# Kernel tuning notes

Measured on AMD Instinct MI355X. Metric: run time of the kernel, lower is better.

## Reference

```python
import jax, jax.numpy as jnp
import numpy as np

N_NODES = 50000
N_EDGES = 500000
IN_FEATS = 64
H_FEATS = 128
NUM_CLASSES = 4
NUM_GRAPHS = 8
NODES_PER_GRAPH = N_NODES // NUM_GRAPHS


def setup_inputs() -> dict:
    key = jax.random.key(0)
    ks = jax.random.split(key, 12)
    in_feat = jax.random.normal(ks[0], (N_NODES, IN_FEATS), dtype=jnp.float32)
    e_weight = jax.random.uniform(ks[1], (N_EDGES,), dtype=jnp.float32)
    src = jax.random.randint(ks[2], (N_EDGES,), 0, N_NODES)
    dst = jax.random.randint(ks[3], (N_EDGES,), 0, N_NODES)
    batch_num_nodes = jnp.full((NUM_GRAPHS,), NODES_PER_GRAPH, dtype=jnp.int64)
    target_node = jax.random.randint(ks[4], (NUM_GRAPHS,), 0, NODES_PER_GRAPH)
    # Glorot-style init for GraphConv weights, zero bias (DGL defaults)
    def glorot(k, fan_in, fan_out):
        s = jnp.sqrt(6.0 / (fan_in + fan_out))
        return jax.random.uniform(k, (fan_in, fan_out), minval=-s, maxval=s, dtype=jnp.float32)
    W1 = glorot(ks[5], IN_FEATS, H_FEATS)
    b1 = jnp.zeros((H_FEATS,), dtype=jnp.float32)
    W2 = glorot(ks[6], H_FEATS, H_FEATS)
    b2 = jnp.zeros((H_FEATS,), dtype=jnp.float32)
    W3 = glorot(ks[7], H_FEATS, NUM_CLASSES)
    b3 = jnp.zeros((NUM_CLASSES,), dtype=jnp.float32)
    return {"in_feat": in_feat, "e_weight": e_weight, "src": src, "dst": dst,
            "batch_num_nodes": batch_num_nodes, "target_node": target_node,
            "W1": W1, "b1": b1, "W2": W2, "b2": b2, "W3": W3, "b3": b3}


def _graph_conv(h, src, dst, e_weight, W, b, out_norm, in_norm, n_nodes):
    # DGL GraphConv, norm='both', with per-edge weights:
    # h_src scaled by out_deg^-1/2, weighted sum over edges into dst,
    # scaled by in_deg^-1/2, then dense transform + bias.
    h = h * out_norm[:, None]
    msg = h[src] * e_weight[:, None]           # [E, d] gather + scale
    agg = jax.ops.segment_sum(msg, dst, num_segments=n_nodes)  # SPMM
    agg = agg * in_norm[:, None]
    return agg @ W + b


def reference(in_feat, e_weight, src, dst, batch_num_nodes, target_node,
              W1, b1, W2, b2, W3, b3):
    n = in_feat.shape[0]
    ones = jnp.ones((src.shape[0],), dtype=in_feat.dtype)
    out_deg = jnp.clip(jax.ops.segment_sum(ones, src, num_segments=n), 1.0)
    in_deg = jnp.clip(jax.ops.segment_sum(ones, dst, num_segments=n), 1.0)
    out_norm = jax.lax.rsqrt(out_deg)
    in_norm = jax.lax.rsqrt(in_deg)

    # target node offsets for batched graphs
    offsets = jnp.concatenate([jnp.zeros((1,), batch_num_nodes.dtype),
                               jnp.cumsum(batch_num_nodes)])[:-1]
    tgt = target_node + offsets

    h = jax.nn.relu(_graph_conv(in_feat, src, dst, e_weight, W1, b1, out_norm, in_norm, n))
    h = jax.nn.relu(_graph_conv(h, src, dst, e_weight, W2, b2, out_norm, in_norm, n))
    h = _graph_conv(h, src, dst, e_weight, W3, b3, out_norm, in_norm, n)
    return h[tgt]
```

## Files before the change

kernel.cpp:

```cpp
#include <hip/hip_runtime.h>

#define NND 50000
#define NED 500000
#define F0 64
#define F1 128
#define NCLS 4
#define NG 8

#define NBLK 256
#define NTHR 1024
#define EPT 2
#define NBAR 8
#define NSUB 8
#define STG 2048
#define STGN 2048
#define BMW ((NND + 31) / 32)
#define EMASK 0x7FFFFu

#define N1CAP 4096
#define N2CAP 1024
#define E1CAP 32768
#define E2CAP 8192
#define E3CAP 2048


template <typename T>
__device__ __forceinline__ void st_wt(T* p, T v) {
    __hip_atomic_store(p, v, __ATOMIC_RELAXED, __HIP_MEMORY_SCOPE_AGENT);
}

__device__ __forceinline__ bool bt(const unsigned* __restrict__ bm, int n) {
    return (bm[n >> 5] >> (n & 31)) & 1u;
}
__device__ __forceinline__ void bset(unsigned* bm, int n) {
    atomicOr(&bm[n >> 5], 1u << (n & 31));
}

__device__ __forceinline__ void load_targets(const int* __restrict__ tnode,
                                             const unsigned* __restrict__ bnn,
                                             int* t) {
    bool is64 = true;
    #pragma unroll
    for (int k = 0; k < 4; k++) if (bnn[2 * k + 1] != 0u) { is64 = false; break; }
    long long off = 0;
    #pragma unroll
    for (int g = 0; g < NG; g++) {
        t[g] = tnode[g] + (int)off;
        off += is64 ? (long long)bnn[2 * g] : (long long)(int)bnn[g];
    }
}

__device__ __forceinline__ int tgt_of(int d, const int* t) {
    int g = -1;
    #pragma unroll
    for (int k = 0; k < NG; k++) if (d == t[k]) g = k;
    return g;
}

__device__ __forceinline__ void gbar(unsigned* bar, int i) {
    asm volatile("s_waitcnt vmcnt(0)" ::: "memory");
    __syncthreads();
    if (threadIdx.x == 0) {
        unsigned* sp = bar + (size_t)(i * (NSUB + 1) + (blockIdx.x & (NSUB - 1))) * 32;
        unsigned* mp = bar + (size_t)(i * (NSUB + 1) + NSUB) * 32;
        unsigned old = __hip_atomic_fetch_add(sp, 1u, __ATOMIC_RELAXED,
                                              __HIP_MEMORY_SCOPE_AGENT);
        if (old + 1u == (unsigned)(NBLK / NSUB))
            __hip_atomic_fetch_add(mp, 1u, __ATOMIC_RELAXED, __HIP_MEMORY_SCOPE_AGENT);
        while (__hip_atomic_load(mp, __ATOMIC_RELAXED, __HIP_MEMORY_SCOPE_AGENT)
               < (unsigned)NSUB)
            __builtin_amdgcn_s_sleep(1);
    }
    __syncthreads();
}

__global__ __launch_bounds__(256) void k_init(char* ws, unsigned zw, unsigned foff, unsigned fw) {
    unsigned t = blockIdx.x * blockDim.x + threadIdx.x;
    if (t < zw) ((uint4*)ws)[t] = make_uint4(0u, 0u, 0u, 0u);
    if (t < fw) ((uint4*)(ws + foff))[t] = make_uint4(~0u, ~0u, ~0u, ~0u);
}

__global__ __launch_bounds__(NTHR) void k_main(
        const float* __restrict__ feat, const float* __restrict__ ew,
        const int* __restrict__ src, const int* __restrict__ dst,
        const int* __restrict__ tnode, const unsigned* __restrict__ bnn,
        const float* __restrict__ W1, const float* __restrict__ b1,
        const float* __restrict__ W2, const float* __restrict__ b2,
        const float* __restrict__ W3, const float* __restrict__ b3,
        float* out,
        int* idx1, int* idx2,
        unsigned* list1, unsigned* list2, unsigned* list3,
        unsigned* cnts, unsigned* incnt, unsigned* outcnt,
        unsigned* bm1, unsigned* bm2, unsigned* bmN,
        float* agg1c, float* agg2c, unsigned* bar) {
    __shared__ unsigned s_le, s_ln, s_eb, s_nb;
    __shared__ unsigned stage[STG];
    __shared__ int stageN[STGN];

    const int tid = threadIdx.x;
    const int gid = blockIdx.x * NTHR + tid;
    const int lane = tid & 63;
    int tg[NG]; load_targets(tnode, bnn, tg);

    {
        if (tid == 0) { s_le = 0; s_ln = 0; }
        __syncthreads();
        int base = gid * EPT;
        if (base < NED) {
            int2 d2 = *(const int2*)(dst + base);
            int dd[2] = {d2.x, d2.y};
            #pragma unroll
            for (int k = 0; k < 2; k++) {
                int d = dd[k];
                int g = tgt_of(d, tg);
                if (g >= 0) {
                    int e = base + k;
                    stage[atomicAdd(&s_le, 1u)] = ((unsigned)g << 19) | (unsigned)e;
                    atomicAdd(&incnt[d], 1u);
                    int s = src[e];
                    bset(bmN, s);
                    if (atomicCAS(&idx2[s], -1, -2) == -1) {
                        bset(bm2, s);
                        stageN[atomicAdd(&s_ln, 1u)] = s;
                    }
                }
            }
        }
        __syncthreads();
        if (tid == 0) {
            s_eb = s_le ? atomicAdd(&cnts[4], s_le) : 0u;
            s_nb = s_ln ? atomicAdd(&cnts[1], s_ln) : 0u;
        }
        __syncthreads();
        for (unsigned t = tid; t < s_le; t += NTHR) {
            unsigned p = s_eb + t; if (p < E3CAP) st_wt(&list3[p], stage[t]);
        }
        for (unsigned t = tid; t < s_ln; t += NTHR) {
            int s = stageN[t]; unsigned id = s_nb + t;
            st_wt(&idx2[s], id < N2CAP ? (int)id : -1);
        }
        if (blockIdx.x == 0 && tid < NG * NCLS) st_wt(&out[tid], b3[tid & 3]);
    }
    gbar(bar, 0);

    {
        if (tid == 0) { s_le = 0; s_ln = 0; }
        __syncthreads();
        int base = gid * EPT;
        if (base < NED) {
            int2 d2 = *(const int2*)(dst + base);
            int dd[2] = {d2.x, d2.y};
            #pragma unroll
            for (int k = 0; k < 2; k++) {
                int d = dd[k];
                if (bt(bm2, d)) {
                    int iv = idx2[d];
                    if (iv >= 0) {
                        int e = base + k;
                        stage[atomicAdd(&s_le, 1u)] = ((unsigned)iv << 19) | (unsigned)e;
                        if (tgt_of(d, tg) < 0) atomicAdd(&incnt[d], 1u);
                        int s = src[e];
                        bset(bmN, s);
                        if (atomicCAS(&idx1[s], -1, -2) == -1) {
                            bset(bm1, s);
                            stageN[atomicAdd(&s_ln, 1u)] = s;
                        }
                    }
                }
            }
        }
        __syncthreads();
        if (tid == 0) {
            s_eb = s_le ? atomicAdd(&cnts[3], s_le) : 0u;
            s_nb = s_ln ? atomicAdd(&cnts[0], s_ln) : 0u;
        }
        __syncthreads();
        for (unsigned t = tid; t < s_le; t += NTHR) {
            unsigned p = s_eb + t; if (p < E2CAP) st_wt(&list2[p], stage[t]);
        }
        for (unsigned t = tid; t < s_ln; t += NTHR) {
            int s = stageN[t]; unsigned id = s_nb + t;
            st_wt(&idx1[s], id < N1CAP ? (int)id : -1);
        }
    }
    gbar(bar, 1);

    {
        if (tid == 0) s_le = 0;
        __syncthreads();
        int base = gid * EPT;
        if (base < NED) {
            int2 d2 = *(const int2*)(dst + base);
            int dd[2] = {d2.x, d2.y};
            #pragma unroll
            for (int k = 0; k < 2; k++) {
                int d = dd[k];
                if (bt(bm1, d)) {
                    int iv = idx1[d];
                    if (iv >= 0) {
                        int e = base + k;
                        stage[atomicAdd(&s_le, 1u)] = ((unsigned)iv << 19) | (unsigned)e;
                        if (idx2[d] < 0 && tgt_of(d, tg) < 0) atomicAdd(&incnt[d], 1u);
                        bset(bmN, src[e]);
                    }
                }
            }
        }
        __syncthreads();
        if (tid == 0) s_eb = s_le ? atomicAdd(&cnts[2], s_le) : 0u;
        __syncthreads();
        for (unsigned t = tid; t < s_le; t += NTHR) {
            unsigned p = s_eb + t; if (p < E1CAP) st_wt(&list1[p], stage[t]);
        }
    }
    gbar(bar, 2);

    {
        int base = gid * EPT;
        if (base < NED) {
            int2 s2 = *(const int2*)(src + base);
            int ss[2] = {s2.x, s2.y};
            #pragma unroll
            for (int k = 0; k < 2; k++)
                if (bt(bmN, ss[k])) atomicAdd(&outcnt[ss[k]], 1u);
        }
    }
    gbar(bar, 3);

    {
        unsigned e1 = cnts[2]; if (e1 > E1CAP) e1 = E1CAP;
        unsigned w = (unsigned)gid >> 6;
        const unsigned nw = (NBLK * NTHR) >> 6;
        for (unsigned i = w; i < e1; i += 2 * nw) {
            unsigned pk0 = list1[i];
            unsigned j2 = i + nw;
            unsigned pk1 = (j2 < e1) ? list1[j2] : 0u;
            int e0 = pk0 & EMASK, i10 = pk0 >> 19;
            float we0 = ew[e0]; int s0 = src[e0];
            int e1i = pk1 & EMASK, i11 = pk1 >> 19;
            float we1 = 0.f; int s1 = 0;
            if (j2 < e1) { we1 = ew[e1i]; s1 = src[e1i]; }
            float wt0 = we0 * rsqrtf(fmaxf((float)outcnt[s0], 1.f));
            atomicAdd(&agg1c[(size_t)i10 * F0 + lane],
                      feat[(size_t)s0 * F0 + lane] * wt0);
            if (j2 < e1) {
                float wt1 = we1 * rsqrtf(fmaxf((float)outcnt[s1], 1.f));
                atomicAdd(&agg1c[(size_t)i11 * F0 + lane],
                          feat[(size_t)s1 * F0 + lane] * wt1);
            }
        }
    }
    gbar(bar, 4);

    {
        unsigned e2 = cnts[3]; if (e2 > E2CAP) e2 = E2CAP;
        unsigned w = (unsigned)gid >> 6;
        const unsigned nw = (NBLK * NTHR) >> 6;
        for (unsigned i = w; i < e2; i += nw) {
            unsigned pk = list2[i];
            int e = pk & EMASK, i2 = pk >> 19;
            float we = ew[e]; int s = src[e];
            int i1 = idx1[s]; if (i1 < 0) continue;
            float wt = we * rsqrtf(fmaxf((float)outcnt[s], 1.f));
            float innorm1 = rsqrtf(fmaxf((float)incnt[s], 1.f));
            float rv = agg1c[(size_t)i1 * F0 + lane];
            float acc0 = 0.f, acc1 = 0.f;
            #pragma unroll 8
            for (int k2 = 0; k2 < F0; k2++) {
                float bv = __shfl(rv, k2, 64);
                acc0 += bv * W1[k2 * F1 + lane];
                acc1 += bv * W1[k2 * F1 + lane + 64];
            }
            float h0 = fmaxf(acc0 * innorm1 + b1[lane], 0.f) * wt;
            float h1v = fmaxf(acc1 * innorm1 + b1[lane + 64], 0.f) * wt;
            atomicAdd(&agg2c[(size_t)i2 * F1 + lane], h0);
            atomicAdd(&agg2c[(size_t)i2 * F1 + lane + 64], h1v);
        }
    }
    gbar(bar, 5);

    {
        unsigned e3 = cnts[4]; if (e3 > E3CAP) e3 = E3CAP;
        unsigned w = (unsigned)gid >> 6;
        const unsigned nw = (NBLK * NTHR) >> 6;
        for (unsigned i = w; i < e3; i += nw) {
            unsigned pk = list3[i];
            int e = pk & EMASK, g = pk >> 19;
            float we = ew[e]; int s = src[e];
            int i2 = idx2[s]; if (i2 < 0) continue;
            float wt = we * rsqrtf(fmaxf((float)outcnt[s], 1.f))
                          * rsqrtf(fmaxf((float)incnt[tg[g]], 1.f));
            float innorm2 = rsqrtf(fmaxf((float)incnt[s], 1.f));
            float rv0 = agg2c[(size_t)i2 * F1 + lane];
            float rv1 = agg2c[(size_t)i2 * F1 + lane + 64];
            float acc0 = 0.f, acc1 = 0.f;
            #pragma unroll 8
            for (int k2 = 0; k2 < 64; k2++) {
                float bv = __shfl(rv0, k2, 64);
                acc0 += bv * W2[k2 * F1 + lane];
                acc1 += bv * W2[k2 * F1 + lane + 64];
            }
            #pragma unroll 8
            for (int k2 = 0; k2 < 64; k2++) {
                float bv = __shfl(rv1, k2, 64);
                acc0 += bv * W2[(k2 + 64) * F1 + lane];
                acc1 += bv * W2[(k2 + 64) * F1 + lane + 64];
            }
            float h20 = fmaxf(acc0 * innorm2 + b2[lane], 0.f);
            float h21 = fmaxf(acc1 * innorm2 + b2[lane + 64], 0.f);
            float oc0 = (h20 * W3[lane * NCLS + 0] + h21 * W3[(lane + 64) * NCLS + 0]) * wt;
            float oc1 = (h20 * W3[lane * NCLS + 1] + h21 * W3[(lane + 64) * NCLS + 1]) * wt;
            float oc2 = (h20 * W3[lane * NCLS + 2] + h21 * W3[(lane + 64) * NCLS + 2]) * wt;
            float oc3 = (h20 * W3[lane * NCLS + 3] + h21 * W3[(lane + 64) * NCLS + 3]) * wt;
            #pragma unroll
            for (int off = 32; off; off >>= 1) {
                oc0 += __shfl_down(oc0, off, 64);
                oc1 += __shfl_down(oc1, off, 64);
                oc2 += __shfl_down(oc2, off, 64);
                oc3 += __shfl_down(oc3, off, 64);
            }
            if (lane == 0) {
                atomicAdd(&out[g * NCLS + 0], oc0);
                atomicAdd(&out[g * NCLS + 1], oc1);
                atomicAdd(&out[g * NCLS + 2], oc2);
                atomicAdd(&out[g * NCLS + 3], oc3);
            }
        }
    }
}

extern "C" void kernel_launch(void* const* d_in, const int* in_sizes, int n_in,
                              void* d_out, int out_size, void* d_ws, size_t ws_size,
                              hipStream_t stream) {
    const float* in_feat = (const float*)d_in[0];
    const float* ew      = (const float*)d_in[1];
    const int*   src     = (const int*)d_in[2];
    const int*   dst     = (const int*)d_in[3];
    const unsigned* bnn  = (const unsigned*)d_in[4];
    const int*   tnode   = (const int*)d_in[5];
    const float* W1 = (const float*)d_in[6];
    const float* b1 = (const float*)d_in[7];
    const float* W2 = (const float*)d_in[8];
    const float* b2 = (const float*)d_in[9];
    const float* W3 = (const float*)d_in[10];
    const float* b3 = (const float*)d_in[11];
    float* out = (float*)d_out;
    (void)in_sizes; (void)n_in; (void)out_size; (void)ws_size;

    char* ws = (char*)d_ws;
    size_t o = 0;
    auto alloc = [&](size_t bytes) { size_t r = o; o += (bytes + 255) & ~(size_t)255; return r; };

    size_t off_outcnt = alloc((size_t)NND * 4);
    size_t off_incnt  = alloc((size_t)NND * 4);
    size_t off_cnts   = alloc(8 * 4);
    size_t off_bar    = alloc((size_t)NBAR * (NSUB + 1) * 32 * 4);
    size_t off_bm1    = alloc((size_t)BMW * 4);
    size_t off_bm2    = alloc((size_t)BMW * 4);
    size_t off_bmN    = alloc((size_t)BMW * 4);
    size_t off_agg1   = alloc((size_t)N1CAP * F0 * 4);
    size_t off_agg2   = alloc((size_t)N2CAP * F1 * 4);
    size_t zero_bytes = o;
    size_t ff_start = o;
    size_t off_idx2   = alloc((size_t)NND * 4);
    size_t off_idx1   = alloc((size_t)NND * 4);
    size_t ff_bytes = o - ff_start;
    size_t off_list3   = alloc((size_t)E3CAP * 4);
    size_t off_list2   = alloc((size_t)E2CAP * 4);
    size_t off_list1   = alloc((size_t)E1CAP * 4);

    unsigned* outcnt  = (unsigned*)(ws + off_outcnt);
    unsigned* incnt   = (unsigned*)(ws + off_incnt);
    unsigned* cnts    = (unsigned*)(ws + off_cnts);
    unsigned* bar     = (unsigned*)(ws + off_bar);
    unsigned* bm1     = (unsigned*)(ws + off_bm1);
    unsigned* bm2     = (unsigned*)(ws + off_bm2);
    unsigned* bmN     = (unsigned*)(ws + off_bmN);
    float*    agg1c   = (float*)(ws + off_agg1);
    float*    agg2c   = (float*)(ws + off_agg2);
    int*      idx2    = (int*)(ws + off_idx2);
    int*      idx1    = (int*)(ws + off_idx1);
    unsigned* list3   = (unsigned*)(ws + off_list3);
    unsigned* list2   = (unsigned*)(ws + off_list2);
    unsigned* list1   = (unsigned*)(ws + off_list1);

    unsigned zw = (unsigned)(zero_bytes / 16);
    unsigned fw = (unsigned)(ff_bytes / 16);
    unsigned iw = zw > fw ? zw : fw;
    k_init<<<(iw + 255) / 256, 256, 0, stream>>>(ws, zw, (unsigned)ff_start, fw);

    k_main<<<NBLK, NTHR, 0, stream>>>(in_feat, ew, src, dst, tnode, bnn,
                                      W1, b1, W2, b2, W3, b3, out,
                                      idx1, idx2, list1, list2, list3,
                                      cnts, incnt, outcnt, bm1, bm2, bmN,
                                      agg1c, agg2c, bar);
}
```

Measured before the change: 61.87 us.

## Halve grid, widen edge loads, and let only tail blocks run final layers

Halves the persistent grid to 128 blocks, with each thread handling 4 edges through int4 loads. After the layer-1 aggregation, only the first 32 blocks continue. The other blocks arrive at the barrier and exit, and later barriers count only those tail blocks. The aim is to cut grid-barrier cost and atomic contention during the small late phases. The risk is less parallelism in the edge scans and the layer-2/3 compute.

```diff
diff --git a/kernel.cpp b/kernel.cpp
--- a/kernel.cpp
+++ b/kernel.cpp
@@ -7,12 +7,13 @@
 #define NCLS 4
 #define NG 8
 
-#define NBLK 256
+#define NBLK 128
 #define NTHR 1024
-#define EPT 2
+#define EPT 4
+#define TAILB 32
 #define NBAR 8
-#define NSUB 8
-#define STG 2048
+#define NSUB 16
+#define STG 4096
 #define STGN 2048
 #define BMW ((NND + 31) / 32)
 #define EMASK 0x7FFFFu
@@ -57,18 +58,34 @@
     return g;
 }
 
+__device__ __forceinline__ void arrive(unsigned* bar, int i) {
+    unsigned* sp = bar + (size_t)(i * (NSUB + 1) + (blockIdx.x & (NSUB - 1))) * 32;
+    unsigned* mp = bar + (size_t)(i * (NSUB + 1) + NSUB) * 32;
+    unsigned old = __hip_atomic_fetch_add(sp, 1u, __ATOMIC_RELAXED,
+                                          __HIP_MEMORY_SCOPE_AGENT);
+    if (old + 1u == (unsigned)(NBLK / NSUB))
+        __hip_atomic_fetch_add(mp, 1u, __ATOMIC_RELAXED, __HIP_MEMORY_SCOPE_AGENT);
+}
+__device__ __forceinline__ void waitfull(unsigned* bar, int i) {
+    unsigned* mp = bar + (size_t)(i * (NSUB + 1) + NSUB) * 32;
+    while (__hip_atomic_load(mp, __ATOMIC_RELAXED, __HIP_MEMORY_SCOPE_AGENT)
+           < (unsigned)NSUB)
+        __builtin_amdgcn_s_sleep(1);
+}
 __device__ __forceinline__ void gbar(unsigned* bar, int i) {
     asm volatile("s_waitcnt vmcnt(0)" ::: "memory");
     __syncthreads();
+    if (threadIdx.x == 0) { arrive(bar, i); waitfull(bar, i); }
+    __syncthreads();
+}
+__device__ __forceinline__ void gbar_tail(unsigned* bar, int i) {
+    asm volatile("s_waitcnt vmcnt(0)" ::: "memory");
+    __syncthreads();
     if (threadIdx.x == 0) {
-        unsigned* sp = bar + (size_t)(i * (NSUB + 1) + (blockIdx.x & (NSUB - 1))) * 32;
         unsigned* mp = bar + (size_t)(i * (NSUB + 1) + NSUB) * 32;
-        unsigned old = __hip_atomic_fetch_add(sp, 1u, __ATOMIC_RELAXED,
-                                              __HIP_MEMORY_SCOPE_AGENT);
-        if (old + 1u == (unsigned)(NBLK / NSUB))
-            __hip_atomic_fetch_add(mp, 1u, __ATOMIC_RELAXED, __HIP_MEMORY_SCOPE_AGENT);
+        __hip_atomic_fetch_add(mp, 1u, __ATOMIC_RELAXED, __HIP_MEMORY_SCOPE_AGENT);
         while (__hip_atomic_load(mp, __ATOMIC_RELAXED, __HIP_MEMORY_SCOPE_AGENT)
-               < (unsigned)NSUB)
+               < (unsigned)TAILB)
             __builtin_amdgcn_s_sleep(1);
     }
     __syncthreads();
@@ -107,10 +124,10 @@
         __syncthreads();
         int base = gid * EPT;
         if (base < NED) {
-            int2 d2 = *(const int2*)(dst + base);
-            int dd[2] = {d2.x, d2.y};
+            int4 d4 = *(const int4*)(dst + base);
+            int dd[4] = {d4.x, d4.y, d4.z, d4.w};
             #pragma unroll
-            for (int k = 0; k < 2; k++) {
+            for (int k = 0; k < 4; k++) {
                 int d = dd[k];
                 int g = tgt_of(d, tg);
                 if (g >= 0) {
@@ -148,10 +165,10 @@
         __syncthreads();
         int base = gid * EPT;
         if (base < NED) {
-            int2 d2 = *(const int2*)(dst + base);
-            int dd[2] = {d2.x, d2.y};
+            int4 d4 = *(const int4*)(dst + base);
+            int dd[4] = {d4.x, d4.y, d4.z, d4.w};
             #pragma unroll
-            for (int k = 0; k < 2; k++) {
+            for (int k = 0; k < 4; k++) {
                 int d = dd[k];
                 if (bt(bm2, d)) {
                     int iv = idx2[d];
@@ -190,10 +207,10 @@
         __syncthreads();
         int base = gid * EPT;
         if (base < NED) {
-            int2 d2 = *(const int2*)(dst + base);
-            int dd[2] = {d2.x, d2.y};
+            int4 d4 = *(const int4*)(dst + base);
+            int dd[4] = {d4.x, d4.y, d4.z, d4.w};
             #pragma unroll
-            for (int k = 0; k < 2; k++) {
+            for (int k = 0; k < 4; k++) {
                 int d = dd[k];
                 if (bt(bm1, d)) {
                     int iv = idx1[d];
@@ -218,10 +235,10 @@
     {
         int base = gid * EPT;
         if (base < NED) {
-            int2 s2 = *(const int2*)(src + base);
-            int ss[2] = {s2.x, s2.y};
+            int4 s4 = *(const int4*)(src + base);
+            int ss[4] = {s4.x, s4.y, s4.z, s4.w};
             #pragma unroll
-            for (int k = 0; k < 2; k++)
+            for (int k = 0; k < 4; k++)
                 if (bt(bmN, ss[k])) atomicAdd(&outcnt[ss[k]], 1u);
         }
     }
@@ -250,12 +267,22 @@
             }
         }
     }
-    gbar(bar, 4);
+    {
+        asm volatile("s_waitcnt vmcnt(0)" ::: "memory");
+        __syncthreads();
+        bool tail = blockIdx.x < TAILB;
+        if (threadIdx.x == 0) {
+            arrive(bar, 4);
+            if (tail) waitfull(bar, 4);
+        }
+        if (!tail) return;
+        __syncthreads();
+    }
 
     {
         unsigned e2 = cnts[3]; if (e2 > E2CAP) e2 = E2CAP;
         unsigned w = (unsigned)gid >> 6;
-        const unsigned nw = (NBLK * NTHR) >> 6;
+        const unsigned nw = (TAILB * NTHR) >> 6;
         for (unsigned i = w; i < e2; i += nw) {
             unsigned pk = list2[i];
             int e = pk & EMASK, i2 = pk >> 19;
@@ -277,12 +304,12 @@
             atomicAdd(&agg2c[(size_t)i2 * F1 + lane + 64], h1v);
         }
     }
-    gbar(bar, 5);
+    gbar_tail(bar, 5);
 
     {
         unsigned e3 = cnts[4]; if (e3 > E3CAP) e3 = E3CAP;
         unsigned w = (unsigned)gid >> 6;
-        const unsigned nw = (NBLK * NTHR) >> 6;
+        const unsigned nw = (TAILB * NTHR) >> 6;
         for (unsigned i = w; i < e3; i += nw) {
             unsigned pk = list3[i];
             int e = pk & EMASK, g = pk >> 19;
```

After: 70.17 us. 13.4% more time.

## Shrink init kernel, replace idx CAS with bitmap claims, shorten tail barriers

Applied to the files above, without the earlier changes.

The init kernel now clears only the small bitmaps, barrier and counter region. The degree counters and aggregation buffers are zeroed inside the main kernel's first phase, and the idx arrays are no longer prefilled with -1, because membership is tracked by atomicOr bitmap claims. The incnt accumulation for target nodes moves into the second pass. After barrier 4, only the first 64 blocks keep running the two small tail aggregation phases, and they sync with a cheaper single-counter barrier while the other blocks exit. This is meant to cut init traffic and grid-wide barrier cost, but it depends on the idx entries being valid whenever their bitmap bit is set and on the in-kernel zeroing finishing before first use.

```diff
diff --git a/kernel.cpp b/kernel.cpp
--- a/kernel.cpp
+++ b/kernel.cpp
@@ -10,7 +10,8 @@
 #define NBLK 256
 #define NTHR 1024
 #define EPT 2
-#define NBAR 8
+#define TAILB 64
+#define NBAR 6
 #define NSUB 8
 #define STG 2048
 #define STGN 2048
@@ -31,6 +32,10 @@
 
 __device__ __forceinline__ bool bt(const unsigned* __restrict__ bm, int n) {
     return (bm[n >> 5] >> (n & 31)) & 1u;
+}
+__device__ __forceinline__ bool bclaim(unsigned* bm, int n) {
+    unsigned old = atomicOr(&bm[n >> 5], 1u << (n & 31));
+    return !(old >> (n & 31) & 1u);
 }
 __device__ __forceinline__ void bset(unsigned* bm, int n) {
     atomicOr(&bm[n >> 5], 1u << (n & 31));
@@ -57,27 +62,42 @@
     return g;
 }
 
+__device__ __forceinline__ void arrive(unsigned* bar, int i) {
+    unsigned* sp = bar + (size_t)(i * (NSUB + 1) + (blockIdx.x & (NSUB - 1))) * 32;
+    unsigned* mp = bar + (size_t)(i * (NSUB + 1) + NSUB) * 32;
+    unsigned old = __hip_atomic_fetch_add(sp, 1u, __ATOMIC_RELAXED,
+                                          __HIP_MEMORY_SCOPE_AGENT);
+    if (old + 1u == (unsigned)(NBLK / NSUB))
+        __hip_atomic_fetch_add(mp, 1u, __ATOMIC_RELAXED, __HIP_MEMORY_SCOPE_AGENT);
+}
+__device__ __forceinline__ void waitfull(unsigned* bar, int i) {
+    unsigned* mp = bar + (size_t)(i * (NSUB + 1) + NSUB) * 32;
+    while (__hip_atomic_load(mp, __ATOMIC_RELAXED, __HIP_MEMORY_SCOPE_AGENT)
+           < (unsigned)NSUB)
+        __builtin_amdgcn_s_sleep(1);
+}
 __device__ __forceinline__ void gbar(unsigned* bar, int i) {
     asm volatile("s_waitcnt vmcnt(0)" ::: "memory");
     __syncthreads();
+    if (threadIdx.x == 0) { arrive(bar, i); waitfull(bar, i); }
+    __syncthreads();
+}
+__device__ __forceinline__ void gbar_tail(unsigned* bar, int i) {
+    asm volatile("s_waitcnt vmcnt(0)" ::: "memory");
+    __syncthreads();
     if (threadIdx.x == 0) {
-        unsigned* sp = bar + (size_t)(i * (NSUB + 1) + (blockIdx.x & (NSUB - 1))) * 32;
         unsigned* mp = bar + (size_t)(i * (NSUB + 1) + NSUB) * 32;
-        unsigned old = __hip_atomic_fetch_add(sp, 1u, __ATOMIC_RELAXED,
-                                              __HIP_MEMORY_SCOPE_AGENT);
-        if (old + 1u == (unsigned)(NBLK / NSUB))
-            __hip_atomic_fetch_add(mp, 1u, __ATOMIC_RELAXED, __HIP_MEMORY_SCOPE_AGENT);
+        __hip_atomic_fetch_add(mp, 1u, __ATOMIC_RELAXED, __HIP_MEMORY_SCOPE_AGENT);
         while (__hip_atomic_load(mp, __ATOMIC_RELAXED, __HIP_MEMORY_SCOPE_AGENT)
-               < (unsigned)NSUB)
+               < (unsigned)TAILB)
             __builtin_amdgcn_s_sleep(1);
     }
     __syncthreads();
 }
 
-__global__ __launch_bounds__(256) void k_init(char* ws, unsigned zw, unsigned foff, unsigned fw) {
+__global__ __launch_bounds__(256) void k_init(char* ws, unsigned zw) {
     unsigned t = blockIdx.x * blockDim.x + threadIdx.x;
     if (t < zw) ((uint4*)ws)[t] = make_uint4(0u, 0u, 0u, 0u);
-    if (t < fw) ((uint4*)(ws + foff))[t] = make_uint4(~0u, ~0u, ~0u, ~0u);
 }
 
 __global__ __launch_bounds__(NTHR) void k_main(
@@ -92,7 +112,8 @@
         unsigned* list1, unsigned* list2, unsigned* list3,
         unsigned* cnts, unsigned* incnt, unsigned* outcnt,
         unsigned* bm1, unsigned* bm2, unsigned* bmN,
-        float* agg1c, float* agg2c, unsigned* bar) {
+        float* agg1c, float* agg2c, unsigned* bar,
+        unsigned long long* zeroA, unsigned zaw) {
     __shared__ unsigned s_le, s_ln, s_eb, s_nb;
     __shared__ unsigned stage[STG];
     __shared__ int stageN[STGN];
@@ -103,6 +124,9 @@
     int tg[NG]; load_targets(tnode, bnn, tg);
 
     {
+        for (unsigned t = (unsigned)gid; t < zaw; t += NBLK * NTHR)
+            st_wt(&zeroA[t], 0ULL);
+
         if (tid == 0) { s_le = 0; s_ln = 0; }
         __syncthreads();
         int base = gid * EPT;
@@ -116,13 +140,9 @@
                 if (g >= 0) {
                     int e = base + k;
                     stage[atomicAdd(&s_le, 1u)] = ((unsigned)g << 19) | (unsigned)e;
-                    atomicAdd(&incnt[d], 1u);
                     int s = src[e];
                     bset(bmN, s);
-                    if (atomicCAS(&idx2[s], -1, -2) == -1) {
-                        bset(bm2, s);
-                        stageN[atomicAdd(&s_ln, 1u)] = s;
-                    }
+                    if (bclaim(bm2, s)) stageN[atomicAdd(&s_ln, 1u)] = s;
                 }
             }
         }
@@ -153,19 +173,16 @@
             #pragma unroll
             for (int k = 0; k < 2; k++) {
                 int d = dd[k];
-                if (bt(bm2, d)) {
-                    int iv = idx2[d];
-                    if (iv >= 0) {
-                        int e = base + k;
-                        stage[atomicAdd(&s_le, 1u)] = ((unsigned)iv << 19) | (unsigned)e;
-                        if (tgt_of(d, tg) < 0) atomicAdd(&incnt[d], 1u);
-                        int s = src[e];
-                        bset(bmN, s);
-                        if (atomicCAS(&idx1[s], -1, -2) == -1) {
-                            bset(bm1, s);
-                            stageN[atomicAdd(&s_ln, 1u)] = s;
-                        }
-                    }
+                int g = tgt_of(d, tg);
+                bool n2ok = false; int iv = -1;
+                if (bt(bm2, d)) { iv = idx2[d]; n2ok = (unsigned)iv < N2CAP; }
+                if (g >= 0 || n2ok) atomicAdd(&incnt[d], 1u);
+                if (n2ok) {
+                    int e = base + k;
+                    stage[atomicAdd(&s_le, 1u)] = ((unsigned)iv << 19) | (unsigned)e;
+                    int s = src[e];
+                    bset(bmN, s);
+                    if (bclaim(bm1, s)) stageN[atomicAdd(&s_ln, 1u)] = s;
                 }
             }
         }
@@ -197,10 +214,10 @@
                 int d = dd[k];
                 if (bt(bm1, d)) {
                     int iv = idx1[d];
-                    if (iv >= 0) {
+                    if ((unsigned)iv < N1CAP) {
                         int e = base + k;
                         stage[atomicAdd(&s_le, 1u)] = ((unsigned)iv << 19) | (unsigned)e;
-                        if (idx2[d] < 0 && tgt_of(d, tg) < 0) atomicAdd(&incnt[d], 1u);
+                        if (!bt(bm2, d) && tgt_of(d, tg) < 0) atomicAdd(&incnt[d], 1u);
                         bset(bmN, src[e]);
                     }
                 }
@@ -250,17 +267,27 @@
             }
         }
     }
-    gbar(bar, 4);
+    {
+        asm volatile("s_waitcnt vmcnt(0)" ::: "memory");
+        __syncthreads();
+        bool tail = blockIdx.x < TAILB;
+        if (threadIdx.x == 0) {
+            arrive(bar, 4);
+            if (tail) waitfull(bar, 4);
+        }
+        if (!tail) return;
+        __syncthreads();
+    }
 
     {
         unsigned e2 = cnts[3]; if (e2 > E2CAP) e2 = E2CAP;
         unsigned w = (unsigned)gid >> 6;
-        const unsigned nw = (NBLK * NTHR) >> 6;
+        const unsigned nw = (TAILB * NTHR) >> 6;
         for (unsigned i = w; i < e2; i += nw) {
             unsigned pk = list2[i];
             int e = pk & EMASK, i2 = pk >> 19;
             float we = ew[e]; int s = src[e];
-            int i1 = idx1[s]; if (i1 < 0) continue;
+            unsigned i1 = (unsigned)idx1[s]; if (i1 >= N1CAP) continue;
             float wt = we * rsqrtf(fmaxf((float)outcnt[s], 1.f));
             float innorm1 = rsqrtf(fmaxf((float)incnt[s], 1.f));
             float rv = agg1c[(size_t)i1 * F0 + lane];
@@ -277,17 +304,17 @@
             atomicAdd(&agg2c[(size_t)i2 * F1 + lane + 64], h1v);
         }
     }
-    gbar(bar, 5);
+    gbar_tail(bar, 5);
 
     {
         unsigned e3 = cnts[4]; if (e3 > E3CAP) e3 = E3CAP;
         unsigned w = (unsigned)gid >> 6;
-        const unsigned nw = (NBLK * NTHR) >> 6;
+        const unsigned nw = (TAILB * NTHR) >> 6;
         for (unsigned i = w; i < e3; i += nw) {
             unsigned pk = list3[i];
             int e = pk & EMASK, g = pk >> 19;
             float we = ew[e]; int s = src[e];
-            int i2 = idx2[s]; if (i2 < 0) continue;
+            unsigned i2 = (unsigned)idx2[s]; if (i2 >= N2CAP) continue;
             float wt = we * rsqrtf(fmaxf((float)outcnt[s], 1.f))
                           * rsqrtf(fmaxf((float)incnt[tg[g]], 1.f));
             float innorm2 = rsqrtf(fmaxf((float)incnt[s], 1.f));
@@ -351,31 +378,31 @@
     size_t o = 0;
     auto alloc = [&](size_t bytes) { size_t r = o; o += (bytes + 255) & ~(size_t)255; return r; };
 
+    size_t off_cnts = alloc(8 * 4);
+    size_t off_bar  = alloc((size_t)NBAR * (NSUB + 1) * 32 * 4);
+    size_t off_bm1  = alloc((size_t)BMW * 4);
+    size_t off_bm2  = alloc((size_t)BMW * 4);
+    size_t off_bmN  = alloc((size_t)BMW * 4);
+    size_t init_bytes = o;
+    size_t zeroA_start = o;
     size_t off_outcnt = alloc((size_t)NND * 4);
     size_t off_incnt  = alloc((size_t)NND * 4);
-    size_t off_cnts   = alloc(8 * 4);
-    size_t off_bar    = alloc((size_t)NBAR * (NSUB + 1) * 32 * 4);
-    size_t off_bm1    = alloc((size_t)BMW * 4);
-    size_t off_bm2    = alloc((size_t)BMW * 4);
-    size_t off_bmN    = alloc((size_t)BMW * 4);
     size_t off_agg1   = alloc((size_t)N1CAP * F0 * 4);
     size_t off_agg2   = alloc((size_t)N2CAP * F1 * 4);
-    size_t zero_bytes = o;
-    size_t ff_start = o;
+    size_t zeroA_bytes = o - zeroA_start;
     size_t off_idx2   = alloc((size_t)NND * 4);
     size_t off_idx1   = alloc((size_t)NND * 4);
-    size_t ff_bytes = o - ff_start;
-    size_t off_list3   = alloc((size_t)E3CAP * 4);
-    size_t off_list2   = alloc((size_t)E2CAP * 4);
-    size_t off_list1   = alloc((size_t)E1CAP * 4);
-
-    unsigned* outcnt  = (unsigned*)(ws + off_outcnt);
-    unsigned* incnt   = (unsigned*)(ws + off_incnt);
+    size_t off_list3  = alloc((size_t)E3CAP * 4);
+    size_t off_list2  = alloc((size_t)E2CAP * 4);
+    size_t off_list1  = alloc((size_t)E1CAP * 4);
+
     unsigned* cnts    = (unsigned*)(ws + off_cnts);
     unsigned* bar     = (unsigned*)(ws + off_bar);
     unsigned* bm1     = (unsigned*)(ws + off_bm1);
     unsigned* bm2     = (unsigned*)(ws + off_bm2);
     unsigned* bmN     = (unsigned*)(ws + off_bmN);
+    unsigned* outcnt  = (unsigned*)(ws + off_outcnt);
+    unsigned* incnt   = (unsigned*)(ws + off_incnt);
     float*    agg1c   = (float*)(ws + off_agg1);
     float*    agg2c   = (float*)(ws + off_agg2);
     int*      idx2    = (int*)(ws + off_idx2);
@@ -384,14 +411,14 @@
     unsigned* list2   = (unsigned*)(ws + off_list2);
     unsigned* list1   = (unsigned*)(ws + off_list1);
 
-    unsigned zw = (unsigned)(zero_bytes / 16);
-    unsigned fw = (unsigned)(ff_bytes / 16);
-    unsigned iw = zw > fw ? zw : fw;
-    k_init<<<(iw + 255) / 256, 256, 0, stream>>>(ws, zw, (unsigned)ff_start, fw);
+    unsigned zw = (unsigned)(init_bytes / 16);
+    k_init<<<(int)((zw + 255) / 256), 256, 0, stream>>>(ws, zw);
 
     k_main<<<NBLK, NTHR, 0, stream>>>(in_feat, ew, src, dst, tnode, bnn,
                                       W1, b1, W2, b2, W3, b3, out,
                                       idx1, idx2, list1, list2, list3,
                                       cnts, incnt, outcnt, bm1, bm2, bmN,
-                                      agg1c, agg2c, bar);
-}
+                                      agg1c, agg2c, bar,
+                                      (unsigned long long*)(ws + zeroA_start),
+                                      (unsigned)(zeroA_bytes / 8));
+}
```

Measured after the change: 62.96 us. About the same (+1.8%).
